# Optimization experiments

Hardware: AMD Instinct MI355X
Metric: run time of the kernel (lower is better)

The kernel has to match this reference:

```python
import jax, jax.numpy as jnp
import numpy as np

B, N, G, E = 4, 8192, 512, 512
D = 3 * E  # fused channel dim = 1536
BN_EPS = 1e-5


def setup_inputs() -> dict:
    key = jax.random.key(0)
    ks = jax.random.split(key, 8)
    f32 = jnp.float32
    return {
        "xyz": jax.random.normal(ks[0], (B, N, 3), f32),
        "centers": jax.random.normal(ks[1], (B, G, 3), f32),
        "H4": jax.random.normal(ks[2], (B, G, E), f32),
        "H8": jax.random.normal(ks[3], (B, G, E), f32),
        "H12": jax.random.normal(ks[4], (B, G, E), f32),
        "w1": jax.random.normal(ks[5], (512, D), f32) * 0.02,
        "b1": jnp.zeros((512,), f32),
        "g1": jnp.ones((512,), f32),
        "be1": jnp.zeros((512,), f32),
        "m1": jnp.zeros((512,), f32),
        "v1": jnp.ones((512,), f32),
        "w2": jax.random.normal(ks[6], (512, 512), f32) * 0.02,
        "b2": jnp.zeros((512,), f32),
        "g2": jnp.ones((512,), f32),
        "be2": jnp.zeros((512,), f32),
        "m2": jnp.zeros((512,), f32),
        "v2": jnp.ones((512,), f32),
    }


def _bn(x, gamma, beta, mean, var):
    # BatchNorm1d, eval mode with running stats (per-channel, last axis)
    return (x - mean) * jax.lax.rsqrt(var + BN_EPS) * gamma + beta


def reference(xyz, centers, H4, H8, H12,
              w1, b1, g1, be1, m1, v1,
              w2, b2, g2, be2, m2, v2):
    fused = jnp.concatenate([H4, H8, H12], axis=-1)  # [B,G,D]
    # squared pairwise distances [B,N,G]
    d = (jnp.sum(xyz * xyz, axis=-1, keepdims=True)
         + jnp.sum(centers * centers, axis=-1)[:, None, :]
         - 2.0 * jnp.einsum('bnc,bgc->bng', xyz, centers))
    neg_d3, idx = jax.lax.top_k(-d, 3)  # 3 smallest distances, ascending
    d3 = -neg_d3  # [B,N,3]
    recip = 1.0 / (d3 + 1e-8)
    w = recip / jnp.sum(recip, axis=-1, keepdims=True)  # [B,N,3]
    # gather neighbor features: [B,N,3,D]
    gathered = jax.vmap(lambda f, i: f[i])(fused, idx)
    interp = jnp.einsum('bnk,bnkd->bnd', w, gathered)  # [B,N,D]
    # 1x1 conv == per-point linear; conv -> BN(eval) -> ReLU, twice
    h = jax.nn.relu(_bn(interp @ w1.T + b1, g1, be1, m1, v1))
    h = jax.nn.relu(_bn(h @ w2.T + b2, g2, be2, m2, v2))
    return h  # [B,N,512]
```

## Files before the change

kernel.cpp:

```cpp
#include <hip/hip_runtime.h>
#include <stdint.h>

#define NP 8192
#define NG 512
#define DF 1536

using f32x4    = __attribute__((ext_vector_type(4))) float;
using bf16x8   = __attribute__((ext_vector_type(8))) __bf16;
using ushort8v = __attribute__((ext_vector_type(8))) unsigned short;


__device__ __forceinline__ unsigned short f32_to_bf16(float f) {
  unsigned int u = __float_as_uint(f);
  u += 0x7fffu + ((u >> 16) & 1u);
  return (unsigned short)(u >> 16);
}
__device__ __forceinline__ float bf2f(unsigned short u) {
  return __uint_as_float(((unsigned)u) << 16);
}

struct FusedArgs {
  const float *xyz, *centers, *H4, *H8, *H12, *w1, *w2;
  const float *g1, *be1, *m1, *v1, *g2, *be2, *m2, *v2, *b1, *b2;
  unsigned short *fswz, *w1s, *w2s, *Amatb;
  int *nidx; float *nw, *s1, *t1, *s2, *t2;
  float *outp;
};

__device__ void phase_knn(const FusedArgs& a, char* smem, int w) {
  const int tid = threadIdx.x;
  float4* cs = (float4*)smem;
  const int b = w >> 7;
  for (int i = tid; i < NG; i += 256) {
    float c0 = a.centers[((size_t)b * NG + i) * 3 + 0];
    float c1 = a.centers[((size_t)b * NG + i) * 3 + 1];
    float c2 = a.centers[((size_t)b * NG + i) * 3 + 2];
    float4 v; v.x = c0; v.y = c1; v.z = c2; v.w = c0 * c0 + c1 * c1 + c2 * c2;
    cs[(i >> 7) * 129 + (i & 127)] = v;
  }
  __syncthreads();
  const int t = (w & 127) * 256 + tid;
  const int p = t >> 2, q = t & 3;
  const size_t pi = (size_t)b * NP + p;
  const float x0 = a.xyz[pi * 3 + 0], x1 = a.xyz[pi * 3 + 1], x2 = a.xyz[pi * 3 + 2];
  const float xx = x0 * x0 + x1 * x1 + x2 * x2;
  float d0 = 3.4e38f, d1 = 3.4e38f, d2 = 3.4e38f;
  int i0 = 0, i1 = 0, i2 = 0;
  const int gbase = q * 128;
  const float4* csq = cs + q * 129;
#pragma unroll 4
  for (int j = 0; j < 128; ++j) {
    float4 c = csq[j];
    float d = xx + c.w - 2.0f * (x0 * c.x + x1 * c.y + x2 * c.z);
    int g = gbase + j;
    bool c0 = d < d0, c1 = d < d1, c2 = d < d2;
    float nd2 = c1 ? d1 : (c2 ? d : d2); int ni2 = c1 ? i1 : (c2 ? g : i2);
    float nd1 = c0 ? d0 : (c1 ? d : d1); int ni1 = c0 ? i0 : (c1 ? g : i1);
    d0 = c0 ? d : d0;                    i0 = c0 ? g : i0;
    d1 = nd1; i1 = ni1; d2 = nd2; i2 = ni2;
  }
#pragma unroll
  for (int off = 1; off <= 2; off <<= 1) {
    float e0 = __shfl_xor(d0, off), e1 = __shfl_xor(d1, off), e2 = __shfl_xor(d2, off);
    int j0 = __shfl_xor(i0, off), j1 = __shfl_xor(i1, off), j2 = __shfl_xor(i2, off);
#pragma unroll
    for (int s = 0; s < 3; ++s) {
      float e = (s == 0) ? e0 : (s == 1 ? e1 : e2);
      int   j = (s == 0) ? j0 : (s == 1 ? j1 : j2);
      bool c0 = (e < d0) || (e == d0 && j < i0);
      bool c1 = (e < d1) || (e == d1 && j < i1);
      bool c2 = (e < d2) || (e == d2 && j < i2);
      float nd2 = c1 ? d1 : (c2 ? e : d2); int ni2 = c1 ? i1 : (c2 ? j : i2);
      float nd1 = c0 ? d0 : (c1 ? e : d1); int ni1 = c0 ? i0 : (c1 ? j : i1);
      d0 = c0 ? e : d0;                    i0 = c0 ? j : i0;
      d1 = nd1; i1 = ni1; d2 = nd2; i2 = ni2;
    }
  }
  if (q == 0) {
    float r0 = 1.0f / (d0 + 1e-8f), r1 = 1.0f / (d1 + 1e-8f), r2 = 1.0f / (d2 + 1e-8f);
    float inv = 1.0f / (r0 + r1 + r2);
    a.nw[pi * 3 + 0] = r0 * inv; a.nw[pi * 3 + 1] = r1 * inv; a.nw[pi * 3 + 2] = r2 * inv;
    a.nidx[pi * 3 + 0] = i0; a.nidx[pi * 3 + 1] = i1; a.nidx[pi * 3 + 2] = i2;
  }
}

__device__ void phase_casts(const FusedArgs& a, int u) {
  const int tid = threadIdx.x;
  if (u < 2048) {
    const int qd = (u - 512) * 256 + tid;
    const int L = qd & 63, t2 = qd >> 6;
    const int kc = t2 % 48, mg = t2 / 48;
    const int m = mg * 16 + (L & 15);
    const int k = kc * 32 + (L >> 4) * 8;
    const float* src = (k < 512) ? a.H4 : (k < 1024 ? a.H8 : a.H12);
    const float* sp = &src[(size_t)m * 512 + (k & 511)];
    float4 va = *(const float4*)sp, vb = *(const float4*)(sp + 4);
    ushort8v o;
    o[0] = f32_to_bf16(va.x); o[1] = f32_to_bf16(va.y);
    o[2] = f32_to_bf16(va.z); o[3] = f32_to_bf16(va.w);
    o[4] = f32_to_bf16(vb.x); o[5] = f32_to_bf16(vb.y);
    o[6] = f32_to_bf16(vb.z); o[7] = f32_to_bf16(vb.w);
    *(ushort8v*)&a.fswz[((size_t)(mg * 48 + kc)) * 512 + L * 8] = o;
  } else if (u < 2432) {
    const int qd = (u - 2048) * 256 + tid;
    const int L = qd & 63, t2 = qd >> 6;
    const int kc = t2 % 48, ng = t2 / 48;
    const int n = ng * 16 + (L & 15);
    const int k = kc * 32 + (L >> 4) * 8;
    const float* sp = &a.w1[(size_t)n * 1536 + k];
    float4 va = *(const float4*)sp, vb = *(const float4*)(sp + 4);
    ushort8v o;
    o[0] = f32_to_bf16(va.x); o[1] = f32_to_bf16(va.y);
    o[2] = f32_to_bf16(va.z); o[3] = f32_to_bf16(va.w);
    o[4] = f32_to_bf16(vb.x); o[5] = f32_to_bf16(vb.y);
    o[6] = f32_to_bf16(vb.z); o[7] = f32_to_bf16(vb.w);
    *(ushort8v*)&a.w1s[((size_t)(ng * 48 + kc)) * 512 + L * 8] = o;
  } else if (u < 2560) {
    const int qd = (u - 2432) * 256 + tid;
    const int L = qd & 63, t2 = qd >> 6;
    const int kc = t2 & 15, ng = t2 >> 4;
    const int n = ng * 16 + (L & 15);
    const int k = kc * 32 + (L >> 4) * 8;
    const float* sp = &a.w2[(size_t)n * 512 + k];
    float4 va = *(const float4*)sp, vb = *(const float4*)(sp + 4);
    ushort8v o;
    o[0] = f32_to_bf16(va.x); o[1] = f32_to_bf16(va.y);
    o[2] = f32_to_bf16(va.z); o[3] = f32_to_bf16(va.w);
    o[4] = f32_to_bf16(vb.x); o[5] = f32_to_bf16(vb.y);
    o[6] = f32_to_bf16(vb.z); o[7] = f32_to_bf16(vb.w);
    *(ushort8v*)&a.w2s[((size_t)(ng * 16 + kc)) * 512 + L * 8] = o;
  } else {
    for (int i = tid; i < 512; i += 256) {
      float sa = a.g1[i] / sqrtf(a.v1[i] + 1e-5f);
      a.s1[i] = sa; a.t1[i] = a.be1[i] - a.m1[i] * sa;
      float sb = a.g2[i] / sqrtf(a.v2[i] + 1e-5f);
      a.s2[i] = sb; a.t2[i] = a.be2[i] - a.m2[i] * sb;
    }
  }
}

__device__ void phase_gemm1(const FusedArgs& a, char* smem, int blk) {
  float* red = (float*)smem;
  const int tid = threadIdx.x, lane = tid & 63, wv = tid >> 6;
  const int m0 = (blk >> 3) * 32;
  const int n0 = (blk & 7) * 64;
  const unsigned short* Ap = a.fswz + ((size_t)(m0 >> 4) * 48 + wv * 12) * 512 + lane * 8;
  const unsigned short* Bp = a.w1s  + ((size_t)(n0 >> 4) * 48 + wv * 12) * 512 + lane * 8;

  f32x4 acc[2][4];
#pragma unroll
  for (int i = 0; i < 2; ++i)
#pragma unroll
    for (int j = 0; j < 4; ++j) acc[i][j] = (f32x4){0.f, 0.f, 0.f, 0.f};

  bf16x8 af[2], bfr[4], afn[2], bfn[4];
#pragma unroll
  for (int i = 0; i < 2; ++i)
    af[i]  = __builtin_bit_cast(bf16x8, *(const ushort8v*)(Ap + (size_t)i * 48 * 512));
#pragma unroll
  for (int i = 0; i < 4; ++i)
    bfr[i] = __builtin_bit_cast(bf16x8, *(const ushort8v*)(Bp + (size_t)i * 48 * 512));
#pragma unroll 1
  for (int kc = 0; kc < 12; ++kc) {
    if (kc < 11) {
#pragma unroll
      for (int i = 0; i < 2; ++i)
        afn[i] = __builtin_bit_cast(bf16x8, *(const ushort8v*)(Ap + (size_t)i * 48 * 512 + (kc + 1) * 512));
#pragma unroll
      for (int i = 0; i < 4; ++i)
        bfn[i] = __builtin_bit_cast(bf16x8, *(const ushort8v*)(Bp + (size_t)i * 48 * 512 + (kc + 1) * 512));
    }
#pragma unroll
    for (int mi = 0; mi < 2; ++mi)
#pragma unroll
      for (int ni = 0; ni < 4; ++ni)
        acc[mi][ni] = __builtin_amdgcn_mfma_f32_16x16x32_bf16(af[mi], bfr[ni], acc[mi][ni], 0, 0, 0);
#pragma unroll
    for (int i = 0; i < 2; ++i) af[i] = afn[i];
#pragma unroll
    for (int i = 0; i < 4; ++i) bfr[i] = bfn[i];
  }

  for (int w = 0; w < 4; ++w) {
    if (wv == w) {
#pragma unroll
      for (int mi = 0; mi < 2; ++mi)
#pragma unroll
        for (int ni = 0; ni < 4; ++ni) {
          int col = ni * 16 + (lane & 15);
#pragma unroll
          for (int r = 0; r < 4; ++r) {
            int row = mi * 16 + (lane >> 4) * 4 + r;
            if (w == 0) red[row * 65 + col] = acc[mi][ni][r];
            else        red[row * 65 + col] += acc[mi][ni][r];
          }
        }
    }
    __syncthreads();
  }
  const int row = tid >> 3;
  const int col = (tid & 7) * 8;
  ushort8v o;
#pragma unroll
  for (int j = 0; j < 8; ++j) {
    int n = n0 + col + j;
    float v = red[row * 65 + col + j];
    o[j] = f32_to_bf16(a.s1[n] * (v + a.b1[n]) + a.t1[n]);
  }
  *(ushort8v*)&a.Amatb[(size_t)(m0 + row) * 512 + n0 + col] = o;
}

__device__ void phase_mega(const FusedArgs& a, char* smem) {
  unsigned short* hl = (unsigned short*)smem;
  const int tid = threadIdx.x, lane = tid & 63, wv = tid >> 6;
  const int xcd = blockIdx.x & 7, slot = blockIdx.x >> 3;
  const int m0 = (xcd * 128 + slot) * 32;

  {
    const int rg = wv >> 1, kc0 = (wv & 1) * 8;
    const int p = m0 + rg * 16 + (lane & 15);
    const int b = p >> 13;
    const int i0 = a.nidx[p * 3 + 0], i1 = a.nidx[p * 3 + 1], i2 = a.nidx[p * 3 + 2];
    const float w0 = a.nw[p * 3 + 0], w1v = a.nw[p * 3 + 1], w2v = a.nw[p * 3 + 2];
    const int co = kc0 * 32 + (lane >> 4) * 8;
    const unsigned short* A0 = a.Amatb + ((size_t)(b * 512 + i0)) * 512 + co;
    const unsigned short* A1 = a.Amatb + ((size_t)(b * 512 + i1)) * 512 + co;
    const unsigned short* A2 = a.Amatb + ((size_t)(b * 512 + i2)) * 512 + co;
    unsigned short* wp = hl + (size_t)(rg * 16 + kc0) * 512 + lane * 8;
#pragma unroll 4
    for (int j = 0; j < 8; ++j) {
      ushort8v u0 = *(const ushort8v*)(A0 + j * 32);
      ushort8v u1 = *(const ushort8v*)(A1 + j * 32);
      ushort8v u2 = *(const ushort8v*)(A2 + j * 32);
      ushort8v o;
#pragma unroll
      for (int jj = 0; jj < 8; ++jj) {
        float v = w0 * bf2f(u0[jj]) + w1v * bf2f(u1[jj]) + w2v * bf2f(u2[jj]);
        o[jj] = f32_to_bf16(fmaxf(v, 0.f));
      }
      *(ushort8v*)(wp + (size_t)j * 512) = o;
    }
  }
  __syncthreads();

  const int n0 = wv * 128;
  const unsigned short* Bbase = a.w2s + (size_t)(n0 >> 4) * 16 * 512 + lane * 8;

  f32x4 acc[2][8];
#pragma unroll
  for (int i = 0; i < 2; ++i)
#pragma unroll
    for (int j = 0; j < 8; ++j) acc[i][j] = (f32x4){0.f, 0.f, 0.f, 0.f};

#pragma unroll 1
  for (int kc = 0; kc < 16; ++kc) {
    bf16x8 af[2];
#pragma unroll
    for (int mi = 0; mi < 2; ++mi)
      af[mi] = __builtin_bit_cast(bf16x8,
          *(const ushort8v*)(hl + (size_t)(mi * 16 + kc) * 512 + lane * 8));
#pragma unroll
    for (int h = 0; h < 2; ++h) {
      bf16x8 bfr[4];
#pragma unroll
      for (int ni = 0; ni < 4; ++ni)
        bfr[ni] = __builtin_bit_cast(bf16x8,
            *(const ushort8v*)(Bbase + (size_t)((h * 4 + ni) * 16 + kc) * 512));
#pragma unroll
      for (int mi = 0; mi < 2; ++mi)
#pragma unroll
        for (int ni = 0; ni < 4; ++ni)
          acc[mi][h * 4 + ni] = __builtin_amdgcn_mfma_f32_16x16x32_bf16(
              af[mi], bfr[ni], acc[mi][h * 4 + ni], 0, 0, 0);
    }
  }

#pragma unroll
  for (int mi = 0; mi < 2; ++mi) {
    int mbase = m0 + mi * 16 + (lane >> 4) * 4;
#pragma unroll
    for (int ni = 0; ni < 8; ++ni) {
      int n = n0 + ni * 16 + (lane & 15);
      float s = a.s2[n], bb = a.b2[n], t = a.t2[n];
      f32x4 v = acc[mi][ni];
#pragma unroll
      for (int r = 0; r < 4; ++r)
        a.outp[(size_t)(mbase + r) * 512 + n] = fmaxf(s * (v[r] + bb) + t, 0.f);
    }
  }
}

__global__ __launch_bounds__(256) void k_prep(FusedArgs a) {
  __shared__ __align__(16) char smem[8448];
  const int u = blockIdx.x;
  if (u < 512) phase_knn(a, smem, u);
  else         phase_casts(a, u);
}
__global__ __launch_bounds__(256) void k_gemm1(FusedArgs a) {
  __shared__ __align__(16) char smem[8448];
  phase_gemm1(a, smem, blockIdx.x);
}
__global__ __launch_bounds__(256, 4) void k_mega(FusedArgs a) {
  __shared__ __align__(16) char smem[32768];
  phase_mega(a, smem);
}

extern "C" void kernel_launch(void* const* d_in, const int* in_sizes, int n_in,
                              void* d_out, int out_size, void* d_ws, size_t ws_size,
                              hipStream_t stream) {
  char* ws = (char*)d_ws;
  FusedArgs a;
  a.xyz     = (const float*)d_in[0];
  a.centers = (const float*)d_in[1];
  a.H4      = (const float*)d_in[2];
  a.H8      = (const float*)d_in[3];
  a.H12     = (const float*)d_in[4];
  a.w1      = (const float*)d_in[5];
  a.b1      = (const float*)d_in[6];
  a.g1      = (const float*)d_in[7];
  a.be1     = (const float*)d_in[8];
  a.m1      = (const float*)d_in[9];
  a.v1      = (const float*)d_in[10];
  a.w2      = (const float*)d_in[11];
  a.b2      = (const float*)d_in[12];
  a.g2      = (const float*)d_in[13];
  a.be2     = (const float*)d_in[14];
  a.m2      = (const float*)d_in[15];
  a.v2      = (const float*)d_in[16];
  a.fswz  = (unsigned short*)(ws);
  a.w1s   = (unsigned short*)(ws + 6291456);
  a.w2s   = (unsigned short*)(ws + 7864320);
  a.Amatb = (unsigned short*)(ws + 8388608);
  a.nidx  = (int*)           (ws + 10485760);
  a.nw    = (float*)         (ws + 10878976);
  a.s1    = (float*)         (ws + 11272192);
  a.t1 = a.s1 + 512; a.s2 = a.t1 + 512; a.t2 = a.s2 + 512;
  a.outp  = (float*)d_out;

  k_prep <<<2561, 256, 0, stream>>>(a);
  k_gemm1<<< 512, 256, 0, stream>>>(a);
  k_mega <<<1024, 256, 0, stream>>>(a);
}
```

Baseline: 170.8 us.

## Overlap KNN with GEMM1, enlarge mega tiles, prefetch B fragments

```diff
diff --git a/kernel.cpp b/kernel.cpp
--- a/kernel.cpp
+++ b/kernel.cpp
@@ -210,14 +210,14 @@
   *(ushort8v*)&a.Amatb[(size_t)(m0 + row) * 512 + n0 + col] = o;
 }
 
-__device__ void phase_mega(const FusedArgs& a, char* smem) {
-  unsigned short* hl = (unsigned short*)smem;
+__global__ __launch_bounds__(512, 4) void k_mega(FusedArgs a) {
+  __shared__ __align__(16) unsigned short hl[64 * 512];
   const int tid = threadIdx.x, lane = tid & 63, wv = tid >> 6;
   const int xcd = blockIdx.x & 7, slot = blockIdx.x >> 3;
-  const int m0 = (xcd * 128 + slot) * 32;
+  const int m0 = (xcd * 64 + slot) * 64;
 
   {
-    const int rg = wv >> 1, kc0 = (wv & 1) * 8;
+    const int rg = wv & 3, kc0 = (wv >> 2) * 8;
     const int p = m0 + rg * 16 + (lane & 15);
     const int b = p >> 13;
     const int i0 = a.nidx[p * 3 + 0], i1 = a.nidx[p * 3 + 1], i2 = a.nidx[p * 3 + 2];
@@ -243,66 +243,66 @@
   }
   __syncthreads();
 
-  const int n0 = wv * 128;
+  const int n0 = wv * 64;
   const unsigned short* Bbase = a.w2s + (size_t)(n0 >> 4) * 16 * 512 + lane * 8;
 
-  f32x4 acc[2][8];
-#pragma unroll
-  for (int i = 0; i < 2; ++i)
-#pragma unroll
-    for (int j = 0; j < 8; ++j) acc[i][j] = (f32x4){0.f, 0.f, 0.f, 0.f};
-
+  f32x4 acc[4][4];
+#pragma unroll
+  for (int i = 0; i < 4; ++i)
+#pragma unroll
+    for (int j = 0; j < 4; ++j) acc[i][j] = (f32x4){0.f, 0.f, 0.f, 0.f};
+
+  bf16x8 bfr[4], bfn[4];
+#pragma unroll
+  for (int ni = 0; ni < 4; ++ni)
+    bfr[ni] = __builtin_bit_cast(bf16x8,
+        *(const ushort8v*)(Bbase + (size_t)(ni * 16) * 512));
 #pragma unroll 1
   for (int kc = 0; kc < 16; ++kc) {
-    bf16x8 af[2];
-#pragma unroll
-    for (int mi = 0; mi < 2; ++mi)
+    if (kc < 15) {
+#pragma unroll
+      for (int ni = 0; ni < 4; ++ni)
+        bfn[ni] = __builtin_bit_cast(bf16x8,
+            *(const ushort8v*)(Bbase + (size_t)(ni * 16 + kc + 1) * 512));
+    }
+    bf16x8 af[4];
+#pragma unroll
+    for (int mi = 0; mi < 4; ++mi)
       af[mi] = __builtin_bit_cast(bf16x8,
           *(const ushort8v*)(hl + (size_t)(mi * 16 + kc) * 512 + lane * 8));
 #pragma unroll
-    for (int h = 0; h < 2; ++h) {
-      bf16x8 bfr[4];
+    for (int mi = 0; mi < 4; ++mi)
 #pragma unroll
       for (int ni = 0; ni < 4; ++ni)
-        bfr[ni] = __builtin_bit_cast(bf16x8,
-            *(const ushort8v*)(Bbase + (size_t)((h * 4 + ni) * 16 + kc) * 512));
-#pragma unroll
-      for (int mi = 0; mi < 2; ++mi)
-#pragma unroll
-        for (int ni = 0; ni < 4; ++ni)
-          acc[mi][h * 4 + ni] = __builtin_amdgcn_mfma_f32_16x16x32_bf16(
-              af[mi], bfr[ni], acc[mi][h * 4 + ni], 0, 0, 0);
-    }
-  }
-
-#pragma unroll
-  for (int mi = 0; mi < 2; ++mi) {
+        acc[mi][ni] = __builtin_amdgcn_mfma_f32_16x16x32_bf16(
+            af[mi], bfr[ni], acc[mi][ni], 0, 0, 0);
+#pragma unroll
+    for (int ni = 0; ni < 4; ++ni) bfr[ni] = bfn[ni];
+  }
+
+#pragma unroll
+  for (int mi = 0; mi < 4; ++mi) {
     int mbase = m0 + mi * 16 + (lane >> 4) * 4;
 #pragma unroll
-    for (int ni = 0; ni < 8; ++ni) {
+    for (int ni = 0; ni < 4; ++ni) {
       int n = n0 + ni * 16 + (lane & 15);
       float s = a.s2[n], bb = a.b2[n], t = a.t2[n];
       f32x4 v = acc[mi][ni];
 #pragma unroll
       for (int r = 0; r < 4; ++r)
-        a.outp[(size_t)(mbase + r) * 512 + n] = fmaxf(s * (v[r] + bb) + t, 0.f);
-    }
-  }
-}
-
-__global__ __launch_bounds__(256) void k_prep(FusedArgs a) {
+        __builtin_nontemporal_store(fmaxf(s * (v[r] + bb) + t, 0.f),
+                                    &a.outp[(size_t)(mbase + r) * 512 + n]);
+    }
+  }
+}
+
+__global__ __launch_bounds__(256) void k_casts(FusedArgs a) {
+  phase_casts(a, 512 + blockIdx.x);
+}
+__global__ __launch_bounds__(256) void k_g1knn(FusedArgs a) {
   __shared__ __align__(16) char smem[8448];
-  const int u = blockIdx.x;
-  if (u < 512) phase_knn(a, smem, u);
-  else         phase_casts(a, u);
-}
-__global__ __launch_bounds__(256) void k_gemm1(FusedArgs a) {
-  __shared__ __align__(16) char smem[8448];
-  phase_gemm1(a, smem, blockIdx.x);
-}
-__global__ __launch_bounds__(256, 4) void k_mega(FusedArgs a) {
-  __shared__ __align__(16) char smem[32768];
-  phase_mega(a, smem);
+  if (blockIdx.x < 512) phase_gemm1(a, smem, blockIdx.x);
+  else                  phase_knn(a, smem, blockIdx.x - 512);
 }
 
 extern "C" void kernel_launch(void* const* d_in, const int* in_sizes, int n_in,
@@ -337,7 +337,7 @@
   a.t1 = a.s1 + 512; a.s2 = a.t1 + 512; a.t2 = a.s2 + 512;
   a.outp  = (float*)d_out;
 
-  k_prep <<<2561, 256, 0, stream>>>(a);
-  k_gemm1<<< 512, 256, 0, stream>>>(a);
-  k_mega <<<1024, 256, 0, stream>>>(a);
-}
+  k_casts<<<2049, 256, 0, stream>>>(a);
+  k_g1knn<<<1024, 256, 0, stream>>>(a);
+  k_mega <<< 512, 512, 0, stream>>>(a);
+}
```

After: 162.4 us. -4.9%, faster.
